# Kernel optimization log

Hardware: AMD Instinct MI355X
Metric: run time of the kernel (lower is better)

## Reference

```python
import jax, jax.numpy as jnp
import numpy as np

S = 1024; VOCAB = 100000; EMB = 300
POS_SZ = 64; CHAR_E = 50; CHAR_ENC = 128; WLEN = 16
NCHARS = 100; NPOSTAG = 50; NPOSITIONS = 1024
D = EMB + 3 * POS_SZ + CHAR_ENC  # word_rep_size = 620
BIH = 128   # per-direction LSTM hidden (bilstm_hidden_size // 2)
TLH = 256; LCC = 128; GCC = 256
NET = 8; NTAGS = 16; NREL = 16
TOKF = 2 * BIH + LCC + TLH       # 640
SENTF = 2 * TOKF + GCC           # 1536

def _p(k, shape):
    return 0.02 * jax.random.normal(k, shape, dtype=jnp.float32)

def setup_inputs():
    key = jax.random.key(0)
    ks = jax.random.split(key, 30)
    return {
        'word_inputs': jax.random.randint(ks[0], (1, S), 0, VOCAB),
        'char_inputs': jax.random.randint(ks[1], (1, S, WLEN), 0, NCHARS),
        'postag_inputs': jax.random.randint(ks[2], (1, S), 0, NPOSTAG),
        'dependency_inputs': jax.random.randint(ks[3], (1, S), 0, 64),
        'position_inputs': jax.random.randint(ks[4], (1, S), 0, NPOSITIONS),
        'topo_order': jnp.arange(S),  # children-before-parents order
        'parent': jnp.concatenate([jnp.arange(1, S), jnp.array([S])]),  # chain dep tree; root -> dummy slot S
        'pointed_token_idx': 5,
        'word_table': _p(ks[5], (VOCAB, EMB)),
        'char_table': _p(ks[6], (NCHARS, CHAR_E)),
        'char_conv_w': _p(ks[7], (CHAR_ENC, CHAR_E, 3)),
        'char_conv_b': jnp.zeros((CHAR_ENC,), jnp.float32),
        'postag_table': _p(ks[8], (NPOSTAG, POS_SZ)),
        'position_table': _p(ks[9], (NPOSITIONS, POS_SZ)),
        'lstm_f_Wx': _p(ks[10], (D, 4 * BIH)),
        'lstm_f_Wh': _p(ks[11], (BIH, 4 * BIH)),
        'lstm_f_b': jnp.zeros((4 * BIH,), jnp.float32),
        'lstm_b_Wx': _p(ks[12], (D, 4 * BIH)),
        'lstm_b_Wh': _p(ks[13], (BIH, 4 * BIH)),
        'lstm_b_b': jnp.zeros((4 * BIH,), jnp.float32),
        'word_cnn_w': _p(ks[14], (LCC, D, 3)),
        'word_cnn_b': jnp.zeros((LCC,), jnp.float32),
        'tl_Wiou': _p(ks[15], (D, 3 * TLH)),
        'tl_Uiou': _p(ks[16], (TLH, 3 * TLH)),
        'tl_biou': jnp.zeros((3 * TLH,), jnp.float32),
        'tl_Wf': _p(ks[17], (D, TLH)),
        'tl_Uf': _p(ks[18], (TLH, TLH)),
        'tl_bf': jnp.zeros((TLH,), jnp.float32),
        'sent_cnn_w': _p(ks[19], (GCC, D, 3)),
        'sent_cnn_b': jnp.zeros((GCC,), jnp.float32),
        'et_w': _p(ks[20], (GCC + TOKF, NET)),
        'et_b': jnp.zeros((NET,), jnp.float32),
        'crf_w': _p(ks[21], (SENTF, NTAGS)),
        'crf_b': jnp.zeros((NTAGS,), jnp.float32),
        'crf_trans': _p(ks[22], (NTAGS, NTAGS)),
        'rel_w': _p(ks[23], (SENTF, NREL)),
        'rel_b': jnp.zeros((NREL,), jnp.float32),
    }

def _conv1d(x, w, b):
    # x: [N, Cin, W], w: [Cout, Cin, K], padding=1 (matches nn.Conv1d(..., padding=1))
    y = jax.lax.conv_general_dilated(x, w, (1,), [(1, 1)], dimension_numbers=('NCW', 'OIW', 'NCW'))
    return y + b[None, :, None]

def _lstm(xs, Wx, Wh, b):
    H = Wh.shape[0]
    def step(carry, x):
        h, c = carry
        g = x @ Wx + h @ Wh + b
        i, f, gg, o = jnp.split(g, 4, axis=-1)
        c = jax.nn.sigmoid(f) * c + jax.nn.sigmoid(i) * jnp.tanh(gg)
        h = jax.nn.sigmoid(o) * jnp.tanh(c)
        return (h, c), h
    init = (jnp.zeros((H,), xs.dtype), jnp.zeros((H,), xs.dtype))
    _, hs = jax.lax.scan(step, init, xs)
    return hs

def _tree_lstm(x, order, parent, Wiou, Uiou, biou, Wf, Uf, bf):
    # ChildSum TreeLSTM over the whole dependency tree in topological order.
    # Equivalent to the source's per-token subtree recursion: each node's h
    # only depends on its subtree.
    Sn, H = x.shape[0], Uf.shape[0]
    xiou = x @ Wiou + biou                 # [S, 3H]
    xf = jnp.concatenate([x @ Wf + bf, jnp.zeros((1, H), x.dtype)], axis=0)  # dummy row for root's parent
    def step(carry, j):
        h, hsum, fcsum = carry
        iou = xiou[j] + hsum[j] @ Uiou
        i, o, u = jnp.split(iou, 3)
        cj = jax.nn.sigmoid(i) * jnp.tanh(u) + fcsum[j]
        hj = jax.nn.sigmoid(o) * jnp.tanh(cj)
        p = parent[j]
        f = jax.nn.sigmoid(xf[p] + hj @ Uf)  # per-child forget gate
        return (h.at[j].set(hj), hsum.at[p].add(hj), fcsum.at[p].add(f * cj)), None
    h0 = jnp.zeros((Sn, H), x.dtype)
    acc0 = jnp.zeros((Sn + 1, H), x.dtype)
    (h, _, _), _ = jax.lax.scan(step, (h0, acc0, acc0), order)
    return h

def _viterbi(emissions, trans):
    # emissions: [S, T]; trans[i, j] = score(i -> j)
    def step(score, e):
        s = score[:, None] + trans
        return jnp.max(s, axis=0) + e, jnp.argmax(s, axis=0)
    final, ptrs = jax.lax.scan(step, emissions[0], emissions[1:])
    last = jnp.argmax(final)
    def bt(tag, p):
        prev = p[tag]
        return prev, prev
    _, prevs = jax.lax.scan(bt, last, ptrs, reverse=True)
    return jnp.concatenate([prevs, last[None]])

def reference(word_inputs, char_inputs, postag_inputs, dependency_inputs, position_inputs, topo_order, parent, pointed_token_idx, word_table, char_table, char_conv_w, char_conv_b, postag_table, position_table, lstm_f_Wx, lstm_f_Wh, lstm_f_b, lstm_b_Wx, lstm_b_Wh, lstm_b_b, word_cnn_w, word_cnn_b, tl_Wiou, tl_Uiou, tl_biou, tl_Wf, tl_Uf, tl_bf, sent_cnn_w, sent_cnn_b, et_w, et_b, crf_w, crf_b, crf_trans, rel_w, rel_b):
    we = word_table[word_inputs]                                   # [1,S,EMB]
    cx = jnp.transpose(char_table[char_inputs[0]], (0, 2, 1))      # [S,CHAR_E,WLEN]
    ce = jnp.max(jax.nn.relu(_conv1d(cx, char_conv_w, char_conv_b)), axis=-1)[None]  # CharCNN -> [1,S,CHAR_ENC]
    pe = postag_table[postag_inputs]
    poe = position_table[position_inputs]
    de = position_table[dependency_inputs]                         # faithful to source bug: uses position table
    inputs = jnp.concatenate([we, ce, pe, poe, de], axis=-1)       # [1,S,D]
    x = inputs[0]
    hf = _lstm(x, lstm_f_Wx, lstm_f_Wh, lstm_f_b)
    hb = _lstm(x[::-1], lstm_b_Wx, lstm_b_Wh, lstm_b_b)[::-1]
    bilstm = jnp.concatenate([hf, hb], axis=-1)[None]              # [1,S,2*BIH]
    xc = jnp.transpose(inputs, (0, 2, 1))                          # [1,D,S]
    local_cnn = jnp.transpose(_conv1d(xc, word_cnn_w, word_cnn_b), (0, 2, 1))
    tree_h = _tree_lstm(x, topo_order, parent, tl_Wiou, tl_Uiou, tl_biou, tl_Wf, tl_Uf, tl_bf)[None]
    global_cnn = jnp.transpose(jnp.max(_conv1d(xc, sent_cnn_w, sent_cnn_b), axis=-1, keepdims=True), (0, 2, 1))  # [1,1,GCC]
    tokens_info = jnp.concatenate([bilstm, local_cnn, tree_h], axis=-1)  # [1,S,TOKF]
    ptr = tokens_info[:, pointed_token_idx, :]                     # [1,TOKF]
    ptr_info = jnp.broadcast_to(ptr[:, None, :], (1, S, TOKF))
    glob_info = jnp.broadcast_to(global_cnn, (1, S, GCC))
    sentence_encoding = jnp.concatenate([tokens_info, ptr_info, glob_info], axis=-1)  # dropout = identity (eval)
    one_vec = jnp.concatenate([global_cnn[:, 0, :], ptr], axis=-1)
    entitytype = jax.nn.softmax(one_vec @ et_w + et_b, axis=-1)
    entities = _viterbi(sentence_encoding[0] @ crf_w + crf_b, crf_trans)
    relations = jax.nn.sigmoid(sentence_encoding @ rel_w + rel_b)
    return sentence_encoding, entitytype, entities, relations
```

## Files before the change

### kernel.cpp

```cpp
#include <hip/hip_runtime.h>
#include <math.h>

#define SEQ   1024
#define DX    620
#define BIH   128
#define TLH   256
#define NTAGS 16

#define O_X      0
#define O_XGF    634880
#define O_XGB    (O_XGF + 524288)
#define O_XIOU   (O_XGB + 524288)
#define O_XF     (O_XIOU + 786432)
#define O_LCNN   (O_XF + 262400)
#define O_SCNN   (O_LCNN + 131072)
#define O_PART   (O_SCNN + 262144)
#define O_GCNN   (O_PART + 4096)
#define O_HF     (O_GCNN + 256)
#define O_HB     (O_HF + 131072)
#define O_TREEH  (O_HB + 131072)
#define O_IOUA   (O_TREEH + 262144)
#define O_FCSUM  (O_IOUA + 787200)
#define O_EMIS   (O_FCSUM + 262400)

#define SENT 0xFFFFFFFFu

__device__ __forceinline__ float sig_f(float x){ return 1.0f/(1.0f + __expf(-x)); }
__device__ __forceinline__ float tanh_f(float x){
  float ax = fabsf(x);
  float e  = __expf(-2.0f*ax);
  float t  = (1.0f - e)/(1.0f + e);
  return x < 0.0f ? -t : t;
}
__device__ __forceinline__ int physslot(int s){ return s ^ ((s>>3)&7); }

__global__ __launch_bounds__(128) void k_embed(
    const int* __restrict__ wi, const int* __restrict__ ci,
    const int* __restrict__ postag_in, const int* __restrict__ dep_in, const int* __restrict__ pos_in,
    const float* __restrict__ word_table, const float* __restrict__ char_table,
    const float* __restrict__ ccw, const float* __restrict__ ccb,
    const float* __restrict__ postag_table, const float* __restrict__ position_table,
    float* __restrict__ x)
{
  int s = blockIdx.x;
  int tid = threadIdx.x;
  __shared__ __align__(16) float ce[50][16];
  for (int idx = tid; idx < 800; idx += 128){
    int e = idx >> 4, t = idx & 15;
    ce[e][t] = char_table[ci[s*16 + t]*50 + e];
  }
  __syncthreads();
  float* xr = x + (size_t)s*DX;
  const float* wrow = word_table + (size_t)wi[s]*300;
  for (int d = tid; d < 300; d += 128) xr[d] = wrow[d];
  {
    int oc = tid;
    const float* wp = ccw + oc*150;
    float acc[16];
    float b = ccb[oc];
    #pragma unroll
    for (int t=0;t<16;t++) acc[t] = b;
    for (int ic=0; ic<50; ic++){
      float w0 = wp[ic*3+0], w1 = wp[ic*3+1], w2 = wp[ic*3+2];
      float cv[16];
      float4 c0 = *(const float4*)&ce[ic][0];
      float4 c1 = *(const float4*)&ce[ic][4];
      float4 c2 = *(const float4*)&ce[ic][8];
      float4 c3 = *(const float4*)&ce[ic][12];
      cv[0]=c0.x;cv[1]=c0.y;cv[2]=c0.z;cv[3]=c0.w;
      cv[4]=c1.x;cv[5]=c1.y;cv[6]=c1.z;cv[7]=c1.w;
      cv[8]=c2.x;cv[9]=c2.y;cv[10]=c2.z;cv[11]=c2.w;
      cv[12]=c3.x;cv[13]=c3.y;cv[14]=c3.z;cv[15]=c3.w;
      #pragma unroll
      for (int t=0;t<16;t++){
        float a = cv[t]*w1;
        if (t > 0)  a += cv[t-1]*w0;
        if (t < 15) a += cv[t+1]*w2;
        acc[t] += a;
      }
    }
    float m = acc[0];
    #pragma unroll
    for (int t=1;t<16;t++) m = fmaxf(m, acc[t]);
    xr[300 + oc] = fmaxf(m, 0.0f);
  }
  if (tid < 64){
    int d = tid;
    xr[428 + d] = postag_table[postag_in[s]*64 + d];
    xr[492 + d] = position_table[pos_in[s]*64 + d];
    xr[556 + d] = position_table[dep_in[s]*64 + d];
  }
}

__device__ __forceinline__ void gemm_tile(
    const float* __restrict__ x, const float* __restrict__ Bm,
    const float* __restrict__ bias, float* __restrict__ C,
    int N, int K, int amode, int bx, int by, int tid,
    float (*As)[64], float (*Bs)[64])
{
  int bn = bx*64, bm = by*64;
  int lane = tid & 63, kg = tid >> 6;
  int tx = tid & 15, ty = tid >> 4;
  float acc[4][4] = {{0.f}};
  for (int k0 = 0; k0 < K; k0 += 20){
    #pragma unroll
    for (int kk=0; kk<5; kk++){
      int k = kg*5 + kk;
      float av;
      if (amode == 0){
        av = x[(size_t)(bm+lane)*DX + k0 + k];
      } else {
        int kc = k0 + k;
        int d  = kc/3;
        int sh = kc - d*3 - 1;
        int row = bm + lane + sh;
        av = (row >= 0 && row < SEQ) ? x[(size_t)row*DX + d] : 0.0f;
      }
      As[k][lane] = av;
      Bs[k][lane] = (amode==0) ? Bm[(size_t)(k0+k)*N + bn + lane]
                               : Bm[(size_t)(bn+lane)*K + k0 + k];
    }
    __syncthreads();
    #pragma unroll
    for (int k=0;k<20;k++){
      float4 a = *(const float4*)&As[k][ty<<2];
      float4 b = *(const float4*)&Bs[k][tx<<2];
      acc[0][0]+=a.x*b.x; acc[0][1]+=a.x*b.y; acc[0][2]+=a.x*b.z; acc[0][3]+=a.x*b.w;
      acc[1][0]+=a.y*b.x; acc[1][1]+=a.y*b.y; acc[1][2]+=a.y*b.z; acc[1][3]+=a.y*b.w;
      acc[2][0]+=a.z*b.x; acc[2][1]+=a.z*b.y; acc[2][2]+=a.z*b.z; acc[2][3]+=a.z*b.w;
      acc[3][0]+=a.w*b.x; acc[3][1]+=a.w*b.y; acc[3][2]+=a.w*b.z; acc[3][3]+=a.w*b.w;
    }
    __syncthreads();
  }
  float4 bb;
  bb.x = bias[bn+(tx<<2)+0]; bb.y = bias[bn+(tx<<2)+1];
  bb.z = bias[bn+(tx<<2)+2]; bb.w = bias[bn+(tx<<2)+3];
  #pragma unroll
  for (int i=0;i<4;i++){
    int row = bm + (ty<<2) + i;
    float4 o;
    o.x = acc[i][0] + bb.x; o.y = acc[i][1] + bb.y;
    o.z = acc[i][2] + bb.z; o.w = acc[i][3] + bb.w;
    *(float4*)&C[(size_t)row*N + bn + (tx<<2)] = o;
  }
}

struct GemmArgs {
  const float* B[4];
  const float* bias[4];
  float*       C[4];
  int N[4]; int K[4];
};

__global__ __launch_bounds__(256) void k_gemm(const float* __restrict__ x, GemmArgs ga)
{
  __shared__ __align__(16) float As[20][64];
  __shared__ __align__(16) float Bs[20][64];
  int z = blockIdx.z;
  if (blockIdx.x*64 >= ga.N[z]) return;
  gemm_tile(x, ga.B[z], ga.bias[z], ga.C[z], ga.N[z], ga.K[z], 0,
            blockIdx.x, blockIdx.y, threadIdx.x, As, Bs);
}

__global__ __launch_bounds__(256) void k_gmax1(const float* __restrict__ scnn, float* __restrict__ part){
  int b = blockIdx.x, c = threadIdx.x;
  float m = -3.0e38f;
  for (int s = b*64; s < b*64 + 64; s++) m = fmaxf(m, scnn[(size_t)s*256 + c]);
  part[b*256 + c] = m;
}
__global__ __launch_bounds__(256) void k_gmax2(const float* __restrict__ part, float* __restrict__ gcnn){
  int c = threadIdx.x;
  float m = -3.0e38f;
  for (int b=0; b<16; b++) m = fmaxf(m, part[b*256 + c]);
  gcnn[c] = m;
}

__global__ __launch_bounds__(256, 1) void k_recur(
    const float* __restrict__ xg_f, const float* __restrict__ xg_b,
    const float* __restrict__ Wh_f, const float* __restrict__ Wh_b,
    const float* __restrict__ xiou, const float* __restrict__ xf,
    const float* __restrict__ Uiou, const float* __restrict__ Uf,
    const int* __restrict__ order, const int* __restrict__ parent,
    float* __restrict__ hf, float* __restrict__ hb,
    float* tree_h, float* iou_acc, float* fcsum,
    const float* __restrict__ x,
    const float* __restrict__ wcnn_w, const float* __restrict__ wcnn_b,
    const float* __restrict__ scnn_w, const float* __restrict__ scnn_b,
    float* __restrict__ lcnn, float* __restrict__ scnn)
{
  int bid = blockIdx.x;
  int tid = threadIdx.x;

  if (bid >= 6){
    __shared__ __align__(16) float As[20][64];
    __shared__ __align__(16) float Bs[20][64];
    int g = bid - 6;
    if (g < 32){
      gemm_tile(x, wcnn_w, wcnn_b, lcnn, 128, 1860, 1, g & 1, g >> 1, tid, As, Bs);
    } else {
      int g2 = g - 32;
      gemm_tile(x, scnn_w, scnn_b, scnn, 256, 1860, 1, g2 & 3, g2 >> 2, tid, As, Bs);
    }
    return;
  }

  if (bid >= 4){
    const float* xg  = (bid == 4) ? xg_f : xg_b;
    const float* Wh  = (bid == 4) ? Wh_f : Wh_b;
    float* hout      = (bid == 4) ? hf : hb;
    int cg = tid >> 1, rg = tid & 1;
    float4 w[4][16];
    #pragma unroll
    for (int cc=0;cc<4;cc++){
      int col = cg*4 + cc;
      #pragma unroll
      for (int r4=0;r4<16;r4++){
        int row = rg*64 + r4*4;
        w[cc][r4].x = Wh[(size_t)(row+0)*512 + col];
        w[cc][r4].y = Wh[(size_t)(row+1)*512 + col];
        w[cc][r4].z = Wh[(size_t)(row+2)*512 + col];
        w[cc][r4].w = Wh[(size_t)(row+3)*512 + col];
      }
    }
    #pragma unroll
    for (int cc=0;cc<4;cc++)
      #pragma unroll
      for (int r4=0;r4<16;r4++)
        asm volatile("" : "+v"(w[cc][r4].x), "+v"(w[cc][r4].y), "+v"(w[cc][r4].z), "+v"(w[cc][r4].w));

    __shared__ __align__(16) float lhl[BIH];
    __shared__ float lcst[BIH];
    __shared__ float gl[512];
    if (tid < BIH){ lhl[tid] = 0.f; lcst[tid] = 0.f; }
    __syncthreads();
    const float4* lhl4 = (const float4*)lhl;
    float4 nxg4 = make_float4(0.f,0.f,0.f,0.f);
    if (rg == 0){
      int n0 = (bid == 4) ? 0 : (SEQ-1);
      nxg4 = *(const float4*)&xg[(size_t)n0*512 + cg*4];
    }
    for (int st=0; st<SEQ; st++){
      int n = (bid == 4) ? st : (SEQ-1-st);
      float4 xg4 = nxg4;
      if (rg == 0 && st+1 < SEQ){
        int n1 = (bid == 4) ? (st+1) : (SEQ-2-st);
        nxg4 = *(const float4*)&xg[(size_t)n1*512 + cg*4];
      }
      float acc[4] = {0.f,0.f,0.f,0.f};
      #pragma unroll
      for (int r4=0;r4<16;r4++){
        float4 h4 = lhl4[rg*16 + r4];
        #pragma unroll
        for (int cc=0;cc<4;cc++)
          acc[cc] += h4.x*w[cc][r4].x + h4.y*w[cc][r4].y + h4.z*w[cc][r4].z + h4.w*w[cc][r4].w;
      }
      #pragma unroll
      for (int cc=0;cc<4;cc++) acc[cc] += __shfl_xor(acc[cc], 1);
      if (rg == 0){
        float4 o = make_float4(acc[0]+xg4.x, acc[1]+xg4.y, acc[2]+xg4.z, acc[3]+xg4.w);
        *(float4*)&gl[cg*4] = o;
      }
      __syncthreads();
      if (tid < BIH){
        float gi = gl[tid], gf = gl[BIH+tid], gg = gl[2*BIH+tid], go = gl[3*BIH+tid];
        float c = sig_f(gf)*lcst[tid] + sig_f(gi)*tanh_f(gg);
        float h = sig_f(go)*tanh_f(c);
        lcst[tid] = c;
        lhl[tid] = h;
        hout[(size_t)n*BIH + tid] = h;
      }
      __syncthreads();
    }
    return;
  }

  int blk = bid;
  int cg = tid >> 3, rg = tid & 7;
  int ulo = blk*64;
  float4 w[8][8];
  #pragma unroll
  for (int cc=0;cc<8;cc++){
    int c = cg*8 + cc;
    const float* Wsrc; size_t stride; int gcol;
    if (c < 192){ Wsrc = Uiou; stride = 768; gcol = (c>>6)*TLH + ulo + (c&63); }
    else        { Wsrc = Uf;   stride = 256; gcol = ulo + (c-192); }
    #pragma unroll
    for (int r4=0;r4<8;r4++){
      int row = rg*32 + r4*4;
      w[cc][r4].x = Wsrc[(size_t)(row+0)*stride + gcol];
      w[cc][r4].y = Wsrc[(size_t)(row+1)*stride + gcol];
      w[cc][r4].z = Wsrc[(size_t)(row+2)*stride + gcol];
      w[cc][r4].w = Wsrc[(size_t)(row+3)*stride + gcol];
    }
  }
  #pragma unroll
  for (int cc=0;cc<8;cc++)
    #pragma unroll
    for (int r4=0;r4<8;r4++)
      asm volatile("" : "+v"(w[cc][r4].x), "+v"(w[cc][r4].y), "+v"(w[cc][r4].z), "+v"(w[cc][r4].w));

  __shared__ __align__(16) float hl[TLH];
  __shared__ float colsum[TLH];
  __shared__ float cprev[64];
  __shared__ int ord_l[SEQ];
  __shared__ int par_l[SEQ];
  for (int i=tid; i<SEQ; i+=256){ ord_l[i] = order[i]; par_l[i] = parent[i]; }
  __syncthreads();
  const float4* hl4 = (const float4*)hl;

  float nxi=0.f, nxo=0.f, nxu=0.f, nxf=0.f;
  if (tid < 64){
    int n0 = ord_l[0];
    int uu = ulo + tid;
    nxi = xiou[(size_t)n0*768 + uu];
    nxo = xiou[(size_t)n0*768 + 256 + uu];
    nxu = xiou[(size_t)n0*768 + 512 + uu];
  }

  for (int t=0; t<SEQ; t++){
    int n  = ord_l[t];
    int m  = (t > 0) ? ord_l[t-1] : 0;
    int pp = (t > 0) ? par_l[m] : -1;
    bool ppeq = (pp == n);

    float xi=nxi, xo=nxo, xu=nxu, xfv=nxf;
    float ac_i=0.f, ac_o=0.f, ac_u=0.f, fcn=0.f;
    float po_i=0.f, po_o=0.f, po_u=0.f, po_f=0.f;
    if (tid < 64){
      int uu = ulo + tid;
      if (t+1 < SEQ){
        int n1 = ord_l[t+1];
        nxi = xiou[(size_t)n1*768 + uu];
        nxo = xiou[(size_t)n1*768 + 256 + uu];
        nxu = xiou[(size_t)n1*768 + 512 + uu];
        nxf = xf[(size_t)par_l[n]*256 + uu];
      }
      ac_i = iou_acc[(size_t)n*768 + uu];
      ac_o = iou_acc[(size_t)n*768 + 256 + uu];
      ac_u = iou_acc[(size_t)n*768 + 512 + uu];
      fcn  = fcsum[(size_t)n*256 + uu];
      if (t > 0 && !ppeq){
        po_i = iou_acc[(size_t)pp*768 + uu];
        po_o = iou_acc[(size_t)pp*768 + 256 + uu];
        po_u = iou_acc[(size_t)pp*768 + 512 + uu];
        po_f = fcsum[(size_t)pp*256 + uu];
      }
    }

    if (t > 0){
      float acc[8] = {0.f,0.f,0.f,0.f,0.f,0.f,0.f,0.f};
      int base = rg << 3;
      #pragma unroll
      for (int r4=0;r4<8;r4++){
        float4 h4 = hl4[base + (r4 ^ rg)];
        #pragma unroll
        for (int cc=0;cc<8;cc++)
          acc[cc] += h4.x*w[cc][r4].x + h4.y*w[cc][r4].y + h4.z*w[cc][r4].z + h4.w*w[cc][r4].w;
      }
      #pragma unroll
      for (int cc=0;cc<8;cc++){
        acc[cc] += __shfl_xor(acc[cc], 1);
        acc[cc] += __shfl_xor(acc[cc], 2);
        acc[cc] += __shfl_xor(acc[cc], 4);
      }
      if (rg == 0){
        *(float4*)&colsum[cg*8]     = make_float4(acc[0], acc[1], acc[2], acc[3]);
        *(float4*)&colsum[cg*8 + 4] = make_float4(acc[4], acc[5], acc[6], acc[7]);
      }
    }
    __syncthreads();

    if (tid < 64){
      int uu = ulo + tid;
      float ai = ac_i, ao = ac_o, au = ac_u, fcs = fcn;
      if (t > 0){
        float vi = colsum[tid], vo = colsum[64+tid], vuu = colsum[128+tid], vf = colsum[192+tid];
        float fg  = sig_f(xfv + vf);
        float fcc = fg * cprev[tid];
        if (ppeq){
          ai += vi; ao += vo; au += vuu; fcs += fcc;
        } else {
          iou_acc[(size_t)pp*768 + uu]       = po_i + vi;
          iou_acc[(size_t)pp*768 + 256 + uu] = po_o + vo;
          iou_acc[(size_t)pp*768 + 512 + uu] = po_u + vuu;
          fcsum[(size_t)pp*256 + uu]         = po_f + fcc;
        }
      }
      float cc = sig_f(xi + ai)*tanh_f(xu + au) + fcs;
      float hh = sig_f(xo + ao)*tanh_f(cc);
      cprev[tid] = cc;
      int s = uu >> 2;
      hl[physslot(s)*4 + (uu & 3)] = hh;
      __hip_atomic_store(&tree_h[(size_t)n*TLH + uu], hh, __ATOMIC_RELAXED, __HIP_MEMORY_SCOPE_AGENT);
    } else {
      int p  = tid - 64;
      int fi = (p < ulo) ? p : p + 64;
      const unsigned* tp = (const unsigned*)(tree_h + (size_t)n*TLH + fi);
      unsigned v = __hip_atomic_load(tp, __ATOMIC_RELAXED, __HIP_MEMORY_SCOPE_AGENT);
      while (v == SENT){
        __builtin_amdgcn_s_sleep(1);
        v = __hip_atomic_load(tp, __ATOMIC_RELAXED, __HIP_MEMORY_SCOPE_AGENT);
      }
      hl[physslot(fi>>2)*4 + (fi&3)] = __uint_as_float(v);
    }
    __syncthreads();
  }
}

__global__ __launch_bounds__(256) void k_assemble(
    const float* __restrict__ hf, const float* __restrict__ hb,
    const float* __restrict__ lcnn, const float* __restrict__ tree_h,
    const float* __restrict__ gcnn,
    const float* __restrict__ crf_w, const float* __restrict__ crf_b,
    const float* __restrict__ rel_w, const float* __restrict__ rel_b,
    const int* __restrict__ ptk,
    float* __restrict__ se_out, float* __restrict__ emis, float* __restrict__ rel_out)
{
  int s = blockIdx.x, tid = threadIdx.x;
  int p = ptk[0];
  __shared__ float se[1536];
  for (int d = tid; d < 1536; d += 256){
    float v;
    if      (d < 128)  v = hf[(size_t)s*128 + d];
    else if (d < 256)  v = hb[(size_t)s*128 + d-128];
    else if (d < 384)  v = lcnn[(size_t)s*128 + d-256];
    else if (d < 640)  v = tree_h[(size_t)s*256 + d-384];
    else if (d < 768)  v = hf[(size_t)p*128 + d-640];
    else if (d < 896)  v = hb[(size_t)p*128 + d-768];
    else if (d < 1024) v = lcnn[(size_t)p*128 + d-896];
    else if (d < 1280) v = tree_h[(size_t)p*256 + d-1024];
    else               v = gcnn[d-1280];
    se[d] = v;
    se_out[(size_t)s*1536 + d] = v;
  }
  __syncthreads();
  int o = tid >> 3, l = tid & 7;
  const float* W = (o < 16) ? crf_w : rel_w;
  int oc = (o < 16) ? o : (o - 16);
  float a = 0.f;
  for (int k = l; k < 1536; k += 8) a += se[k]*W[(size_t)k*16 + oc];
  for (int off = 4; off; off >>= 1) a += __shfl_down(a, off, 8);
  if (l == 0){
    if (o < 16) emis[(size_t)s*16 + o] = a + crf_b[o];
    else        rel_out[(size_t)s*16 + oc] = sig_f(a + rel_b[oc]);
  }
}

__global__ __launch_bounds__(256) void k_entity(
    const float* __restrict__ hf, const float* __restrict__ hb,
    const float* __restrict__ lcnn, const float* __restrict__ tree_h,
    const float* __restrict__ gcnn,
    const float* __restrict__ et_w, const float* __restrict__ et_b,
    const int* __restrict__ ptk, float* __restrict__ out_et)
{
  __shared__ float ov[896];
  __shared__ float lg[8];
  int tid = threadIdx.x;
  int p = ptk[0];
  for (int d = tid; d < 896; d += 256){
    float v;
    if      (d < 256) v = gcnn[d];
    else if (d < 384) v = hf[(size_t)p*128 + d-256];
    else if (d < 512) v = hb[(size_t)p*128 + d-384];
    else if (d < 640) v = lcnn[(size_t)p*128 + d-512];
    else              v = tree_h[(size_t)p*256 + d-640];
    ov[d] = v;
  }
  __syncthreads();
  int o = tid >> 5, l = tid & 31;
  float a = 0.f;
  for (int k = l; k < 896; k += 32) a += ov[k]*et_w[(size_t)k*8 + o];
  for (int off = 16; off; off >>= 1) a += __shfl_down(a, off, 32);
  if (l == 0) lg[o] = a + et_b[o];
  __syncthreads();
  if (tid == 0){
    float mx = lg[0];
    for (int i=1;i<8;i++) mx = fmaxf(mx, lg[i]);
    float e[8], sum = 0.f;
    for (int i=0;i<8;i++){ e[i] = __expf(lg[i]-mx); sum += e[i]; }
    for (int i=0;i<8;i++) out_et[i] = e[i]/sum;
  }
}

__global__ __launch_bounds__(64) void k_viterbi(
    const float* __restrict__ emis, const float* __restrict__ trans, float* __restrict__ out_e)
{
  __shared__ __align__(16) float ring[64][16];
  __shared__ unsigned char ptrs[1023*16];
  __shared__ float scL[16];
  int l = threadIdx.x;
  int j = l >> 2, iq = l & 3;
  float tr0 = trans[(iq*4+0)*16 + j];
  float tr1 = trans[(iq*4+1)*16 + j];
  float tr2 = trans[(iq*4+2)*16 + j];
  float tr3 = trans[(iq*4+3)*16 + j];
  {
    const float* src = &emis[(size_t)l*16];
    float4 a = *(const float4*)(src+0), b = *(const float4*)(src+4);
    float4 c = *(const float4*)(src+8), d = *(const float4*)(src+12);
    *(float4*)&ring[l][0] = a;  *(float4*)&ring[l][4] = b;
    *(float4*)&ring[l][8] = c;  *(float4*)&ring[l][12] = d;
  }
  float cur = ring[0][j];
  float sc0 = __shfl(cur, (iq*4+0)<<2, 64);
  float sc1 = __shfl(cur, (iq*4+1)<<2, 64);
  float sc2 = __shfl(cur, (iq*4+2)<<2, 64);
  float sc3 = __shfl(cur, (iq*4+3)<<2, 64);
  float myfinal = cur;
  for (int t=1; t<1024; t++){
    if ((t & 63) == 0){
      const float* src = &emis[(size_t)(t+l)*16];
      float4 a = *(const float4*)(src+0), b = *(const float4*)(src+4);
      float4 c = *(const float4*)(src+8), d = *(const float4*)(src+12);
      int rr = (t+l) & 63;
      *(float4*)&ring[rr][0] = a;  *(float4*)&ring[rr][4] = b;
      *(float4*)&ring[rr][8] = c;  *(float4*)&ring[rr][12] = d;
    }
    float v0 = sc0 + tr0, v1 = sc1 + tr1, v2 = sc2 + tr2, v3 = sc3 + tr3;
    float best = v0; int barg = iq*4;
    if (v1 > best){ best = v1; barg = iq*4+1; }
    if (v2 > best){ best = v2; barg = iq*4+2; }
    if (v3 > best){ best = v3; barg = iq*4+3; }
    float ob = __shfl_down(best, 1, 4); int oa = __shfl_down(barg, 1, 4);
    if (ob > best){ best = ob; barg = oa; }
    ob = __shfl_down(best, 2, 4); oa = __shfl_down(barg, 2, 4);
    if (ob > best){ best = ob; barg = oa; }
    float ns = 0.f;
    if (iq == 0){
      ns = best + ring[t & 63][j];
      ptrs[(t-1)*16 + j] = (unsigned char)barg;
      myfinal = ns;
    }
    sc0 = __shfl(ns, (iq*4+0)<<2, 64);
    sc1 = __shfl(ns, (iq*4+1)<<2, 64);
    sc2 = __shfl(ns, (iq*4+2)<<2, 64);
    sc3 = __shfl(ns, (iq*4+3)<<2, 64);
  }
  if (iq == 0) scL[j] = myfinal;
  if (l == 0){
    float b = scL[0]; int last = 0;
    #pragma unroll
    for (int i=1;i<16;i++){ if (scL[i] > b){ b = scL[i]; last = i; } }
    out_e[1023] = (float)last;
    int cur2 = last;
    for (int t=1022; t>=0; t--){ cur2 = (int)ptrs[t*16 + cur2]; out_e[t] = (float)cur2; }
  }
}

extern "C" void kernel_launch(void* const* d_in, const int* in_sizes, int n_in,
                              void* d_out, int out_size, void* d_ws, size_t ws_size,
                              hipStream_t stream)
{
  (void)in_sizes; (void)n_in; (void)out_size; (void)ws_size;
  const int*   wi         = (const int*)d_in[0];
  const int*   ci         = (const int*)d_in[1];
  const int*   postag_in  = (const int*)d_in[2];
  const int*   dep_in     = (const int*)d_in[3];
  const int*   pos_in     = (const int*)d_in[4];
  const int*   order      = (const int*)d_in[5];
  const int*   parent     = (const int*)d_in[6];
  const int*   ptk        = (const int*)d_in[7];
  const float* word_table = (const float*)d_in[8];
  const float* char_table = (const float*)d_in[9];
  const float* ccw        = (const float*)d_in[10];
  const float* ccb        = (const float*)d_in[11];
  const float* postag_tab = (const float*)d_in[12];
  const float* pos_tab    = (const float*)d_in[13];
  const float* Wx_f       = (const float*)d_in[14];
  const float* Wh_f       = (const float*)d_in[15];
  const float* b_f        = (const float*)d_in[16];
  const float* Wx_b       = (const float*)d_in[17];
  const float* Wh_b       = (const float*)d_in[18];
  const float* b_b        = (const float*)d_in[19];
  const float* wcnn_w     = (const float*)d_in[20];
  const float* wcnn_b     = (const float*)d_in[21];
  const float* Wiou       = (const float*)d_in[22];
  const float* Uiou       = (const float*)d_in[23];
  const float* biou       = (const float*)d_in[24];
  const float* Wf_t       = (const float*)d_in[25];
  const float* Uf_t       = (const float*)d_in[26];
  const float* bf_t       = (const float*)d_in[27];
  const float* scnn_w     = (const float*)d_in[28];
  const float* scnn_b     = (const float*)d_in[29];
  const float* et_w       = (const float*)d_in[30];
  const float* et_b       = (const float*)d_in[31];
  const float* crf_w      = (const float*)d_in[32];
  const float* crf_b      = (const float*)d_in[33];
  const float* crf_trans  = (const float*)d_in[34];
  const float* rel_w      = (const float*)d_in[35];
  const float* rel_b      = (const float*)d_in[36];

  float* ws = (float*)d_ws;
  float* x      = ws + O_X;
  float* xg_f   = ws + O_XGF;
  float* xg_b   = ws + O_XGB;
  float* xiou   = ws + O_XIOU;
  float* xf     = ws + O_XF;
  float* lcnn   = ws + O_LCNN;
  float* scnn   = ws + O_SCNN;
  float* part   = ws + O_PART;
  float* gcnn   = ws + O_GCNN;
  float* hf     = ws + O_HF;
  float* hb     = ws + O_HB;
  float* tree_h = ws + O_TREEH;
  float* iou_acc= ws + O_IOUA;
  float* fcsum  = ws + O_FCSUM;
  float* emis   = ws + O_EMIS;

  float* outF     = (float*)d_out;
  float* se_out   = outF;
  float* et_out   = outF + 1572864;
  float* ent_out  = outF + 1572872;
  float* rel_out  = outF + 1573896;

  hipMemsetAsync(xf, 0, (size_t)1025*256*sizeof(float), stream);
  hipMemsetAsync(iou_acc, 0, ((size_t)1025*768 + 1025*256)*sizeof(float), stream);
  hipMemsetAsync(tree_h, 0xFF, (size_t)1024*256*sizeof(float), stream);

  k_embed<<<SEQ, 128, 0, stream>>>(wi, ci, postag_in, dep_in, pos_in,
                                   word_table, char_table, ccw, ccb,
                                   postag_tab, pos_tab, x);

  GemmArgs ga;
  ga.B[0]=Wx_f;  ga.bias[0]=b_f;   ga.C[0]=xg_f; ga.N[0]=512; ga.K[0]=620;
  ga.B[1]=Wx_b;  ga.bias[1]=b_b;   ga.C[1]=xg_b; ga.N[1]=512; ga.K[1]=620;
  ga.B[2]=Wiou;  ga.bias[2]=biou;  ga.C[2]=xiou; ga.N[2]=768; ga.K[2]=620;
  ga.B[3]=Wf_t;  ga.bias[3]=bf_t;  ga.C[3]=xf;   ga.N[3]=256; ga.K[3]=620;
  k_gemm<<<dim3(12,16,4), 256, 0, stream>>>(x, ga);

  k_recur<<<102, 256, 0, stream>>>(xg_f, xg_b, Wh_f, Wh_b, xiou, xf, Uiou, Uf_t,
                                   order, parent, hf, hb, tree_h, iou_acc, fcsum,
                                   x, wcnn_w, wcnn_b, scnn_w, scnn_b, lcnn, scnn);

  k_gmax1<<<16, 256, 0, stream>>>(scnn, part);
  k_gmax2<<<1, 256, 0, stream>>>(part, gcnn);

  k_assemble<<<SEQ, 256, 0, stream>>>(hf, hb, lcnn, tree_h, gcnn,
                                      crf_w, crf_b, rel_w, rel_b, ptk,
                                      se_out, emis, rel_out);

  k_entity<<<1, 256, 0, stream>>>(hf, hb, lcnn, tree_h, gcnn, et_w, et_b, ptk, et_out);

  k_viterbi<<<1, 64, 0, stream>>>(emis, crf_trans, ent_out);
}
```

Measured before the change: 2.762 ms.

## Fuse input-projection GEMMs into recurrent kernel with per-row-block ready counters

Removes the separate k_gemm launch and computes the LSTM and tree-LSTM input projections inside k_recur, on 256 extra worker blocks. Workers store tiles with agent-scope atomic stores and bump per-(matrix,row-block) counters. The recurrent blocks spin-wait on those counters before reading each 64-row chunk, so the serial recurrences can start before the whole projection finishes. The CNN tiles are regrouped three per block, and launch bounds change to allow two blocks per CU. The risk is deadlock or stalls if the spinning blocks occupy resources before the producer blocks are scheduled, and the atomic scalar stores write less efficiently than the previous float4 stores.

```diff
diff --git a/kernel.cpp b/kernel.cpp
--- a/kernel.cpp
+++ b/kernel.cpp
@@ -22,6 +22,7 @@
 #define O_IOUA   (O_TREEH + 262144)
 #define O_FCSUM  (O_IOUA + 787200)
 #define O_EMIS   (O_FCSUM + 262400)
+#define O_CNT    (O_EMIS + 16384)
 
 #define SENT 0xFFFFFFFFu
 
@@ -96,7 +97,7 @@
     const float* __restrict__ x, const float* __restrict__ Bm,
     const float* __restrict__ bias, float* __restrict__ C,
     int N, int K, int amode, int bx, int by, int tid,
-    float (*As)[64], float (*Bs)[64])
+    float (*As)[64], float (*Bs)[64], int agentc)
 {
   int bn = bx*64, bm = by*64;
   int lane = tid & 63, kg = tid >> 6;
@@ -138,28 +139,18 @@
   #pragma unroll
   for (int i=0;i<4;i++){
     int row = bm + (ty<<2) + i;
-    float4 o;
-    o.x = acc[i][0] + bb.x; o.y = acc[i][1] + bb.y;
-    o.z = acc[i][2] + bb.z; o.w = acc[i][3] + bb.w;
-    *(float4*)&C[(size_t)row*N + bn + (tx<<2)] = o;
-  }
-}
-
-struct GemmArgs {
-  const float* B[4];
-  const float* bias[4];
-  float*       C[4];
-  int N[4]; int K[4];
-};
-
-__global__ __launch_bounds__(256) void k_gemm(const float* __restrict__ x, GemmArgs ga)
-{
-  __shared__ __align__(16) float As[20][64];
-  __shared__ __align__(16) float Bs[20][64];
-  int z = blockIdx.z;
-  if (blockIdx.x*64 >= ga.N[z]) return;
-  gemm_tile(x, ga.B[z], ga.bias[z], ga.C[z], ga.N[z], ga.K[z], 0,
-            blockIdx.x, blockIdx.y, threadIdx.x, As, Bs);
+    float v0 = acc[i][0]+bb.x, v1 = acc[i][1]+bb.y, v2 = acc[i][2]+bb.z, v3 = acc[i][3]+bb.w;
+    if (agentc){
+      float* p = &C[(size_t)row*N + bn + (tx<<2)];
+      __hip_atomic_store(p+0, v0, __ATOMIC_RELAXED, __HIP_MEMORY_SCOPE_AGENT);
+      __hip_atomic_store(p+1, v1, __ATOMIC_RELAXED, __HIP_MEMORY_SCOPE_AGENT);
+      __hip_atomic_store(p+2, v2, __ATOMIC_RELAXED, __HIP_MEMORY_SCOPE_AGENT);
+      __hip_atomic_store(p+3, v3, __ATOMIC_RELAXED, __HIP_MEMORY_SCOPE_AGENT);
+    } else {
+      float4 o; o.x=v0; o.y=v1; o.z=v2; o.w=v3;
+      *(float4*)&C[(size_t)row*N + bn + (tx<<2)] = o;
+    }
+  }
 }
 
 __global__ __launch_bounds__(256) void k_gmax1(const float* __restrict__ scnn, float* __restrict__ part){
@@ -175,7 +166,14 @@
   gcnn[c] = m;
 }
 
-__global__ __launch_bounds__(256, 1) void k_recur(
+struct RGemm {
+  const float* B[4];
+  const float* bias[4];
+  float*       C[4];
+  int          N[4];
+};
+
+__global__ __launch_bounds__(256, 2) void k_recur(
     const float* __restrict__ xg_f, const float* __restrict__ xg_b,
     const float* __restrict__ Wh_f, const float* __restrict__ Wh_b,
     const float* __restrict__ xiou, const float* __restrict__ xf,
@@ -183,23 +181,46 @@
     const int* __restrict__ order, const int* __restrict__ parent,
     float* __restrict__ hf, float* __restrict__ hb,
     float* tree_h, float* iou_acc, float* fcsum,
-    const float* __restrict__ x,
+    const float* __restrict__ x, RGemm rg_args,
     const float* __restrict__ wcnn_w, const float* __restrict__ wcnn_b,
     const float* __restrict__ scnn_w, const float* __restrict__ scnn_b,
-    float* __restrict__ lcnn, float* __restrict__ scnn)
+    float* __restrict__ lcnn, float* __restrict__ scnn,
+    int* cnt)
 {
   int bid = blockIdx.x;
   int tid = threadIdx.x;
 
+  if (bid >= 262){
+    __shared__ __align__(16) float As[20][64];
+    __shared__ __align__(16) float Bs[20][64];
+    int j = bid - 262;
+    for (int s=0;s<3;s++){
+      int tn = j*3 + s;
+      if (tn < 32) gemm_tile(x, wcnn_w, wcnn_b, lcnn, 128, 1860, 1, tn&1, tn>>1, tid, As, Bs, 0);
+      else { int t2 = tn-32; gemm_tile(x, scnn_w, scnn_b, scnn, 256, 1860, 1, t2&3, t2>>2, tid, As, Bs, 0); }
+      __syncthreads();
+    }
+    return;
+  }
+
   if (bid >= 6){
     __shared__ __align__(16) float As[20][64];
     __shared__ __align__(16) float Bs[20][64];
-    int g = bid - 6;
-    if (g < 32){
-      gemm_tile(x, wcnn_w, wcnn_b, lcnn, 128, 1860, 1, g & 1, g >> 1, tid, As, Bs);
-    } else {
-      int g2 = g - 32;
-      gemm_tile(x, scnn_w, scnn_b, scnn, 256, 1860, 1, g2 & 3, g2 >> 2, tid, As, Bs);
+    int j = bid - 6;
+    for (int s=0;s<2;s++){
+      int T = j*2 + s;
+      int k = T>>5, r = T&31;
+      int z, by, bn;
+      if (r < 8)       { z=0; by=k;    bn=r;    }
+      else if (r < 16) { z=1; by=15-k; bn=r-8;  }
+      else if (r < 28) { z=2; by=k;    bn=r-16; }
+      else             { z=3; by=k;    bn=r-28; }
+      gemm_tile(x, rg_args.B[z], rg_args.bias[z], rg_args.C[z], rg_args.N[z],
+                620, 0, bn, by, tid, As, Bs, 1);
+      __syncthreads();
+      if (tid == 0)
+        __hip_atomic_fetch_add(&cnt[z*16 + by], 1, __ATOMIC_RELEASE, __HIP_MEMORY_SCOPE_AGENT);
+      __syncthreads();
     }
     return;
   }
@@ -208,6 +229,7 @@
     const float* xg  = (bid == 4) ? xg_f : xg_b;
     const float* Wh  = (bid == 4) ? Wh_f : Wh_b;
     float* hout      = (bid == 4) ? hf : hb;
+    int zc = (bid == 4) ? 0 : 1;
     int cg = tid >> 1, rg = tid & 1;
     float4 w[4][16];
     #pragma unroll
@@ -234,6 +256,22 @@
     if (tid < BIH){ lhl[tid] = 0.f; lcst[tid] = 0.f; }
     __syncthreads();
     const float4* lhl4 = (const float4*)lhl;
+
+    int Wm = (bid == 4) ? -1 : 16;
+    {
+      int n0 = (bid == 4) ? 0 : (SEQ-1);
+      int g0 = n0 >> 6;
+      if (bid == 4){
+        for (int g = Wm+1; g <= g0; g++)
+          while (__hip_atomic_load(&cnt[zc*16+g], __ATOMIC_ACQUIRE, __HIP_MEMORY_SCOPE_AGENT) < 8)
+            __builtin_amdgcn_s_sleep(8);
+      } else {
+        for (int g = Wm-1; g >= g0; g--)
+          while (__hip_atomic_load(&cnt[zc*16+g], __ATOMIC_ACQUIRE, __HIP_MEMORY_SCOPE_AGENT) < 8)
+            __builtin_amdgcn_s_sleep(8);
+      }
+      Wm = g0;
+    }
     float4 nxg4 = make_float4(0.f,0.f,0.f,0.f);
     if (rg == 0){
       int n0 = (bid == 4) ? 0 : (SEQ-1);
@@ -242,9 +280,25 @@
     for (int st=0; st<SEQ; st++){
       int n = (bid == 4) ? st : (SEQ-1-st);
       float4 xg4 = nxg4;
-      if (rg == 0 && st+1 < SEQ){
+      if (st+1 < SEQ){
         int n1 = (bid == 4) ? (st+1) : (SEQ-2-st);
-        nxg4 = *(const float4*)&xg[(size_t)n1*512 + cg*4];
+        int g1 = n1 >> 6;
+        if (bid == 4){
+          if (g1 > Wm){
+            for (int g = Wm+1; g <= g1; g++)
+              while (__hip_atomic_load(&cnt[zc*16+g], __ATOMIC_ACQUIRE, __HIP_MEMORY_SCOPE_AGENT) < 8)
+                __builtin_amdgcn_s_sleep(8);
+            Wm = g1;
+          }
+        } else {
+          if (g1 < Wm){
+            for (int g = Wm-1; g >= g1; g--)
+              while (__hip_atomic_load(&cnt[zc*16+g], __ATOMIC_ACQUIRE, __HIP_MEMORY_SCOPE_AGENT) < 8)
+                __builtin_amdgcn_s_sleep(8);
+            Wm = g1;
+          }
+        }
+        if (rg == 0) nxg4 = *(const float4*)&xg[(size_t)n1*512 + cg*4];
       }
       float acc[4] = {0.f,0.f,0.f,0.f};
       #pragma unroll
@@ -308,9 +362,18 @@
   __syncthreads();
   const float4* hl4 = (const float4*)hl;
 
+  int Wm = -1;
   float nxi=0.f, nxo=0.f, nxu=0.f, nxf=0.f;
   if (tid < 64){
     int n0 = ord_l[0];
+    int need = n0 >> 6;
+    for (int g = 0; g <= need; g++){
+      while (__hip_atomic_load(&cnt[32+g], __ATOMIC_ACQUIRE, __HIP_MEMORY_SCOPE_AGENT) < 12)
+        __builtin_amdgcn_s_sleep(8);
+      while (__hip_atomic_load(&cnt[48+g], __ATOMIC_ACQUIRE, __HIP_MEMORY_SCOPE_AGENT) < 4)
+        __builtin_amdgcn_s_sleep(8);
+    }
+    Wm = need;
     int uu = ulo + tid;
     nxi = xiou[(size_t)n0*768 + uu];
     nxo = xiou[(size_t)n0*768 + 256 + uu];
@@ -330,10 +393,22 @@
       int uu = ulo + tid;
       if (t+1 < SEQ){
         int n1 = ord_l[t+1];
+        int pr = par_l[n];
+        int need = n1 >> 6;
+        if (pr < SEQ && (pr>>6) > need) need = pr>>6;
+        if (need > Wm){
+          for (int g = Wm+1; g <= need; g++){
+            while (__hip_atomic_load(&cnt[32+g], __ATOMIC_ACQUIRE, __HIP_MEMORY_SCOPE_AGENT) < 12)
+              __builtin_amdgcn_s_sleep(8);
+            while (__hip_atomic_load(&cnt[48+g], __ATOMIC_ACQUIRE, __HIP_MEMORY_SCOPE_AGENT) < 4)
+              __builtin_amdgcn_s_sleep(8);
+          }
+          Wm = need;
+        }
         nxi = xiou[(size_t)n1*768 + uu];
         nxo = xiou[(size_t)n1*768 + 256 + uu];
         nxu = xiou[(size_t)n1*768 + 512 + uu];
-        nxf = xf[(size_t)par_l[n]*256 + uu];
+        nxf = xf[(size_t)pr*256 + uu];
       }
       ac_i = iou_acc[(size_t)n*768 + uu];
       ac_o = iou_acc[(size_t)n*768 + 256 + uu];
@@ -606,6 +681,7 @@
   float* iou_acc= ws + O_IOUA;
   float* fcsum  = ws + O_FCSUM;
   float* emis   = ws + O_EMIS;
+  int*   cnt    = (int*)(ws + O_CNT);
 
   float* outF     = (float*)d_out;
   float* se_out   = outF;
@@ -616,21 +692,22 @@
   hipMemsetAsync(xf, 0, (size_t)1025*256*sizeof(float), stream);
   hipMemsetAsync(iou_acc, 0, ((size_t)1025*768 + 1025*256)*sizeof(float), stream);
   hipMemsetAsync(tree_h, 0xFF, (size_t)1024*256*sizeof(float), stream);
+  hipMemsetAsync(cnt, 0, 256, stream);
 
   k_embed<<<SEQ, 128, 0, stream>>>(wi, ci, postag_in, dep_in, pos_in,
                                    word_table, char_table, ccw, ccb,
                                    postag_tab, pos_tab, x);
 
-  GemmArgs ga;
-  ga.B[0]=Wx_f;  ga.bias[0]=b_f;   ga.C[0]=xg_f; ga.N[0]=512; ga.K[0]=620;
-  ga.B[1]=Wx_b;  ga.bias[1]=b_b;   ga.C[1]=xg_b; ga.N[1]=512; ga.K[1]=620;
-  ga.B[2]=Wiou;  ga.bias[2]=biou;  ga.C[2]=xiou; ga.N[2]=768; ga.K[2]=620;
-  ga.B[3]=Wf_t;  ga.bias[3]=bf_t;  ga.C[3]=xf;   ga.N[3]=256; ga.K[3]=620;
-  k_gemm<<<dim3(12,16,4), 256, 0, stream>>>(x, ga);
-
-  k_recur<<<102, 256, 0, stream>>>(xg_f, xg_b, Wh_f, Wh_b, xiou, xf, Uiou, Uf_t,
+  RGemm rga;
+  rga.B[0]=Wx_f;  rga.bias[0]=b_f;   rga.C[0]=xg_f; rga.N[0]=512;
+  rga.B[1]=Wx_b;  rga.bias[1]=b_b;   rga.C[1]=xg_b; rga.N[1]=512;
+  rga.B[2]=Wiou;  rga.bias[2]=biou;  rga.C[2]=xiou; rga.N[2]=768;
+  rga.B[3]=Wf_t;  rga.bias[3]=bf_t;  rga.C[3]=xf;   rga.N[3]=256;
+
+  k_recur<<<294, 256, 0, stream>>>(xg_f, xg_b, Wh_f, Wh_b, xiou, xf, Uiou, Uf_t,
                                    order, parent, hf, hb, tree_h, iou_acc, fcsum,
-                                   x, wcnn_w, wcnn_b, scnn_w, scnn_b, lcnn, scnn);
+                                   x, rga, wcnn_w, wcnn_b, scnn_w, scnn_b, lcnn, scnn,
+                                   cnt);
 
   k_gmax1<<<16, 256, 0, stream>>>(scnn, part);
   k_gmax2<<<1, 256, 0, stream>>>(part, gcnn);
```

Result: slower. 7.238 ms (+162.1%).
